# Kernel tuning notes

Hardware: AMD Instinct MI355X
Metric: run time of the kernel (lower is better)

Reference implementation:

```python
import jax, jax.numpy as jnp
import numpy as np

MIN_STD = 0.01
FOURIER_SCALE = 20.0


def _grid_sample_bilinear(h_flat, gx, gy):
    """Bilinear grid_sample with align_corners=True.
    h_flat: (N, C, H, W); gx, gy: (N, P) in [-1, 1].
    Returns (N, P, C)."""
    N, C, H, W = h_flat.shape
    x = (gx + 1.0) * 0.5 * (W - 1)
    y = (gy + 1.0) * 0.5 * (H - 1)
    x0 = jnp.clip(jnp.floor(x), 0, W - 1)
    y0 = jnp.clip(jnp.floor(y), 0, H - 1)
    x1 = jnp.clip(x0 + 1, 0, W - 1)
    y1 = jnp.clip(y0 + 1, 0, H - 1)
    wx = x - x0
    wy = y - y0
    x0i, x1i = x0.astype(jnp.int32), x1.astype(jnp.int32)
    y0i, y1i = y0.astype(jnp.int32), y1.astype(jnp.int32)
    hf = h_flat.reshape(N, C, H * W)  # flatten spatial for gather

    def gather(yi, xi):
        idx = (yi * W + xi)[:, None, :]  # (N,1,P)
        return jnp.take_along_axis(hf, idx, axis=2)  # (N,C,P)

    v00 = gather(y0i, x0i)
    v01 = gather(y0i, x1i)
    v10 = gather(y1i, x0i)
    v11 = gather(y1i, x1i)
    wx_ = wx[:, None, :]
    wy_ = wy[:, None, :]
    top = v00 * (1 - wx_) + v01 * wx_
    bot = v10 * (1 - wx_) + v11 * wx_
    out = top * (1 - wy_) + bot * wy_  # (N,C,P)
    return out.transpose(0, 2, 1)  # (N,P,C)


def setup_inputs() -> dict:
    key = jax.random.key(0)
    ks = jax.random.split(key, 9)
    B, T, C, Hg, Wg, P = 8, 16, 128, 64, 64, 2048
    h_dim, fmap = 128, 128
    in_dim = h_dim + 2 * fmap  # 384
    h_grid = jax.random.normal(ks[0], (B, T, C, Hg, Wg), dtype=jnp.float32)
    xs = jax.random.uniform(ks[1], (B, T, P, 1), dtype=jnp.float32)
    ys = jax.random.uniform(ks[2], (B, T, P, 1), dtype=jnp.float32)
    B_mat = jax.random.normal(ks[3], (2, fmap), dtype=jnp.float32) * FOURIER_SCALE
    W0 = jax.random.normal(ks[4], (in_dim, h_dim), dtype=jnp.float32) / np.sqrt(in_dim)
    b0 = jnp.zeros((h_dim,), dtype=jnp.float32)
    W1 = jax.random.normal(ks[5], (h_dim, h_dim), dtype=jnp.float32) / np.sqrt(h_dim)
    b1 = jnp.zeros((h_dim,), dtype=jnp.float32)
    W2 = jax.random.normal(ks[6], (h_dim, 2), dtype=jnp.float32) / np.sqrt(h_dim)
    b2 = jnp.zeros((2,), dtype=jnp.float32)
    return {"h_grid": h_grid, "xs": xs, "ys": ys, "B_mat": B_mat,
            "W0": W0, "b0": b0, "W1": W1, "b1": b1, "W2": W2, "b2": b2}


def reference(h_grid, xs, ys, B_mat, W0, b0, W1, b1, W2, b2):
    B, T, P, _ = xs.shape
    _, _, C, Hg, Wg = h_grid.shape
    h_flat = h_grid.reshape(B * T, C, Hg, Wg)
    coords = jnp.concatenate([xs, ys], axis=-1).reshape(B * T, P, 2)
    # map [spatial_min, spatial_max]=[0,1] to [-1,1]
    g = 2.0 * coords - 1.0
    sampled = _grid_sample_bilinear(h_flat, g[..., 0], g[..., 1])  # (BT,P,C)
    # Fourier features: [sin(2pi x B), cos(2pi x B)]
    proj = 2.0 * jnp.pi * jnp.einsum('npd,df->npf', coords, B_mat)
    spatial = jnp.concatenate([jnp.sin(proj), jnp.cos(proj)], axis=-1)  # (BT,P,256)
    x = jnp.concatenate([sampled, spatial], axis=-1)  # (BT,P,384)
    x = jax.nn.relu(x @ W0 + b0)
    x = jax.nn.relu(x @ W1 + b1)
    out = (x @ W2 + b2).reshape(B, T, P, 2)
    mu = out[..., 0:1]
    sigma = jax.nn.softplus(out[..., 1:2]) + MIN_STD
    return jnp.concatenate([mu, sigma], axis=-1)  # (B,T,P,2)
```

## Files before the change

kernel.cpp:

```cpp
#include <hip/hip_runtime.h>
#include <hip/hip_bf16.h>
#include <math.h>

typedef __attribute__((ext_vector_type(8))) short short8;
typedef __attribute__((ext_vector_type(4))) float f32x4;
typedef __attribute__((ext_vector_type(4))) unsigned short us4;

__device__ __forceinline__ float b2f(unsigned short u) {
    union { unsigned int i; float f; } v; v.i = ((unsigned int)u) << 16; return v.f;
}
__device__ __forceinline__ unsigned short f2b(float f) {
    __hip_bfloat16 h = __float2bfloat16(f);
    return *reinterpret_cast<unsigned short*>(&h);
}

__global__ __launch_bounds__(256) void transpose_h(const float* __restrict__ hg,
                                                   unsigned short* __restrict__ ht) {
    __shared__ float t[128][65];
    int bid = blockIdx.x;
    int x = bid & 7, r = bid >> 3;
    int n = x * 16 + (r & 15);
    int pb = r >> 4;
    int tid = threadIdx.x;
    const float* src = hg + (size_t)n * 128 * 4096 + pb * 64;
    int j = tid & 63, i0 = tid >> 6;
#pragma unroll
    for (int ii = 0; ii < 32; ++ii) {
        int ch = ii * 4 + i0;
        t[ch][j] = src[(size_t)ch * 4096 + j];
    }
    __syncthreads();
#pragma unroll
    for (int it = 0; it < 8; ++it) {
        int idx = tid + it * 256;
        int px = idx >> 5, cq = idx & 31;
        us4 o;
#pragma unroll
        for (int rr = 0; rr < 4; ++rr) o[rr] = f2b(t[cq * 4 + rr][px]);
        *(us4*)&ht[((size_t)n * 4096 + pb * 64 + px) * 128 + cq * 4] = o;
    }
}

__global__ void prep_weights(const float* __restrict__ W0, const float* __restrict__ W1,
                             const float* __restrict__ W2,
                             unsigned short* __restrict__ w0t, unsigned short* __restrict__ w1t,
                             unsigned short* __restrict__ w2p) {
    int i = blockIdx.x * 256 + threadIdx.x;
    const int total0 = 128 * 384, total1 = 128 * 128, total2 = 16 * 128;
    for (int idx = i; idx < total0; idx += gridDim.x * 256) {
        int j = idx / 384, k = idx - j * 384;
        w0t[idx] = f2b(W0[k * 128 + j]);
    }
    for (int idx = i; idx < total1; idx += gridDim.x * 256) {
        int j = idx >> 7, k = idx & 127;
        w1t[idx] = f2b(W1[k * 128 + j]);
    }
    for (int idx = i; idx < total2; idx += gridDim.x * 256) {
        int r = idx >> 7, k = idx & 127;
        w2p[idx] = (r < 2) ? f2b(W2[k * 2 + r]) : (unsigned short)0;
    }
}

#define W0P 784
#define HBP 272
#define MFMA_BF16 __builtin_amdgcn_mfma_f32_16x16x32_bf16

__global__ __launch_bounds__(512, 2) void fused_decoder(
    const unsigned short* __restrict__ ht,
    const float* __restrict__ xs, const float* __restrict__ ys,
    const float* __restrict__ Bm,
    const unsigned short* __restrict__ w0t, const float* __restrict__ b0,
    const unsigned short* __restrict__ w1t, const float* __restrict__ b1,
    const unsigned short* __restrict__ w2p, const float* __restrict__ b2,
    float* __restrict__ out)
{
    __shared__ char smem[128 * W0P + 8 * 16 * HBP];
    char* w0s = smem;
    int tid = threadIdx.x, lane = tid & 63, w = tid >> 6;
    int lr = lane & 15, lg = lane >> 4;
    char* hb = smem + 128 * W0P + w * 16 * HBP;

    {
        const short8* src = (const short8*)w0t;
#pragma unroll 1
        for (int it = 0; it < 12; ++it) {
            int c = tid + it * 512;
            int row = c / 48, cc = c - row * 48;
            *(short8*)(w0s + row * W0P + cc * 16) = src[c];
        }
    }
    __syncthreads();

    int bid = blockIdx.x;
    int x = bid & 7, s = bid >> 3;
    int n = x * 16 + (s >> 3);
    int pt = s & 7;
    int gp0 = n * 2048 + pt * 256 + w * 32;

    float xm[2], ym[2], wxv[2], wyv[2];
    int o00[2], o01[2], o10[2], o11[2];
#pragma unroll
    for (int m = 0; m < 2; ++m) {
        int gp = gp0 + m * 16 + lr;
        float xc = xs[gp], yc = ys[gp];
        xm[m] = xc; ym[m] = yc;
        float px = xc * 63.f, py = yc * 63.f;
        float x0f = fminf(fmaxf(floorf(px), 0.f), 63.f);
        float y0f = fminf(fmaxf(floorf(py), 0.f), 63.f);
        wxv[m] = px - x0f; wyv[m] = py - y0f;
        int xi0 = (int)x0f, yi0 = (int)y0f;
        int xi1 = min(xi0 + 1, 63), yi1 = min(yi0 + 1, 63);
        o00[m] = (yi0 * 64 + xi0) * 256;
        o01[m] = (yi0 * 64 + xi1) * 256;
        o10[m] = (yi1 * 64 + xi0) * 256;
        o11[m] = (yi1 * 64 + xi1) * 256;
    }
    const char* base = (const char*)ht + ((size_t)n << 20) + lg * 16;

    f32x4 acc[2][8];
#pragma unroll
    for (int nj = 0; nj < 8; ++nj) {
        float bv = b0[nj * 16 + lr];
        acc[0][nj] = (f32x4){bv, bv, bv, bv};
        acc[1][nj] = acc[0][nj];
    }

    short8 c00[2], c01[2], c10[2], c11[2];
#pragma unroll
    for (int m = 0; m < 2; ++m) {
        c00[m] = *(const short8*)(base + o00[m]);
        c01[m] = *(const short8*)(base + o01[m]);
        c10[m] = *(const short8*)(base + o10[m]);
        c11[m] = *(const short8*)(base + o11[m]);
    }

#pragma unroll 1
    for (int q = 0; q < 4; ++q) {
        short8 asn[2], acs[2];
        {
            int f0 = q * 32 + lg * 8;
            f32x4 B0a = *(const f32x4*)&Bm[f0];
            f32x4 B0b = *(const f32x4*)&Bm[f0 + 4];
            f32x4 B1a = *(const f32x4*)&Bm[128 + f0];
            f32x4 B1b = *(const f32x4*)&Bm[128 + f0 + 4];
#pragma unroll
            for (int m = 0; m < 2; ++m) {
                float t_[8];
#pragma unroll
                for (int j = 0; j < 4; ++j) {
                    t_[j]     = xm[m] * B0a[j] + ym[m] * B1a[j];
                    t_[4 + j] = xm[m] * B0b[j] + ym[m] * B1b[j];
                }
#pragma unroll
                for (int j = 0; j < 8; ++j) {
                    float tf = t_[j] - floorf(t_[j]);
                    float sv, cv;
                    asm("v_sin_f32 %0, %1" : "=v"(sv) : "v"(tf));
                    asm("v_cos_f32 %0, %1" : "=v"(cv) : "v"(tf));
                    asn[m][j] = (short)f2b(sv);
                    acs[m][j] = (short)f2b(cv);
                }
            }
        }
#pragma unroll
        for (int nj = 0; nj < 8; ++nj) {
            short8 bs = *(const short8*)(w0s + (nj * 16 + lr) * W0P + (4 + q) * 64 + lg * 16);
            acc[0][nj] = MFMA_BF16(asn[0], bs, acc[0][nj], 0, 0, 0);
            acc[1][nj] = MFMA_BF16(asn[1], bs, acc[1][nj], 0, 0, 0);
        }
#pragma unroll
        for (int nj = 0; nj < 8; ++nj) {
            short8 bc = *(const short8*)(w0s + (nj * 16 + lr) * W0P + (8 + q) * 64 + lg * 16);
            acc[0][nj] = MFMA_BF16(acs[0], bc, acc[0][nj], 0, 0, 0);
            acc[1][nj] = MFMA_BF16(acs[1], bc, acc[1][nj], 0, 0, 0);
        }

        short8 a[2];
#pragma unroll
        for (int m = 0; m < 2; ++m) {
            float wx = wxv[m], wy = wyv[m];
            float ivx = 1.f - wx, ivy = 1.f - wy;
#pragma unroll
            for (int j = 0; j < 8; ++j) {
                float top = b2f((unsigned short)c00[m][j]) * ivx + b2f((unsigned short)c01[m][j]) * wx;
                float bot = b2f((unsigned short)c10[m][j]) * ivx + b2f((unsigned short)c11[m][j]) * wx;
                a[m][j] = (short)f2b(top * ivy + bot * wy);
            }
        }
        if (q < 3) {
            int so = (q + 1) * 64;
#pragma unroll
            for (int m = 0; m < 2; ++m) {
                c00[m] = *(const short8*)(base + o00[m] + so);
                c01[m] = *(const short8*)(base + o01[m] + so);
                c10[m] = *(const short8*)(base + o10[m] + so);
                c11[m] = *(const short8*)(base + o11[m] + so);
            }
        }
#pragma unroll
        for (int nj = 0; nj < 8; ++nj) {
            short8 b = *(const short8*)(w0s + (nj * 16 + lr) * W0P + q * 64 + lg * 16);
            acc[0][nj] = MFMA_BF16(a[0], b, acc[0][nj], 0, 0, 0);
            acc[1][nj] = MFMA_BF16(a[1], b, acc[1][nj], 0, 0, 0);
        }
    }

    float bb2 = (lr < 2) ? b2[lr] : 0.f;
#pragma unroll
    for (int m = 0; m < 2; ++m) {
#pragma unroll
        for (int nj = 0; nj < 8; ++nj)
#pragma unroll
            for (int r = 0; r < 4; ++r) {
                int row = lg * 4 + r;
                *(unsigned short*)(hb + row * HBP + (nj * 16 + lr) * 2) =
                    f2b(fmaxf(acc[m][nj][r], 0.f));
            }
        asm volatile("s_waitcnt lgkmcnt(0)" ::: "memory");
        short8 a1[4];
#pragma unroll
        for (int ks = 0; ks < 4; ++ks)
            a1[ks] = *(const short8*)(hb + lr * HBP + ks * 64 + lg * 16);
        asm volatile("s_waitcnt lgkmcnt(0)" ::: "memory");

#pragma unroll
        for (int nj = 0; nj < 8; ++nj) {
            float bv = b1[nj * 16 + lr];
            acc[m][nj] = (f32x4){bv, bv, bv, bv};
        }
#pragma unroll
        for (int ks = 0; ks < 4; ++ks)
#pragma unroll
            for (int nj = 0; nj < 8; ++nj) {
                short8 b = *(const short8*)&w1t[(nj * 16 + lr) * 128 + ks * 32 + lg * 8];
                acc[m][nj] = MFMA_BF16(a1[ks], b, acc[m][nj], 0, 0, 0);
            }

#pragma unroll
        for (int nj = 0; nj < 8; ++nj)
#pragma unroll
            for (int r = 0; r < 4; ++r) {
                int row = lg * 4 + r;
                *(unsigned short*)(hb + row * HBP + (nj * 16 + lr) * 2) =
                    f2b(fmaxf(acc[m][nj][r], 0.f));
            }
        asm volatile("s_waitcnt lgkmcnt(0)" ::: "memory");

        f32x4 acc2 = (f32x4){bb2, bb2, bb2, bb2};
#pragma unroll
        for (int ks = 0; ks < 4; ++ks) {
            short8 a2 = *(const short8*)(hb + lr * HBP + ks * 64 + lg * 16);
            short8 bz = *(const short8*)&w2p[lr * 128 + ks * 32 + lg * 8];
            acc2 = MFMA_BF16(a2, bz, acc2, 0, 0, 0);
        }
        asm volatile("s_waitcnt lgkmcnt(0)" ::: "memory");
        if (lr < 2) {
#pragma unroll
            for (int r = 0; r < 4; ++r) {
                int gpo = gp0 + m * 16 + lg * 4 + r;
                float v = acc2[r];
                if (lr == 0) {
                    out[gpo * 2] = v;
                } else {
                    float sp = (v > 20.f) ? v : log1pf(expf(v));
                    out[gpo * 2 + 1] = sp + 0.01f;
                }
            }
        }
    }
}

extern "C" void kernel_launch(void* const* d_in, const int* in_sizes, int n_in,
                              void* d_out, int out_size, void* d_ws, size_t ws_size,
                              hipStream_t stream) {
    const float* h_grid = (const float*)d_in[0];
    const float* xs = (const float*)d_in[1];
    const float* ys = (const float*)d_in[2];
    const float* Bm = (const float*)d_in[3];
    const float* W0 = (const float*)d_in[4];
    const float* b0 = (const float*)d_in[5];
    const float* W1 = (const float*)d_in[6];
    const float* b1 = (const float*)d_in[7];
    const float* W2 = (const float*)d_in[8];
    const float* b2 = (const float*)d_in[9];
    float* out = (float*)d_out;

    unsigned short* ht  = (unsigned short*)d_ws;
    unsigned short* w0t = (unsigned short*)((char*)d_ws + 134217728ull);
    unsigned short* w1t = w0t + 128 * 384;
    unsigned short* w2p = w1t + 128 * 128;

    transpose_h<<<dim3(8192), dim3(256), 0, stream>>>(h_grid, ht);
    prep_weights<<<dim3(64), dim3(256), 0, stream>>>(W0, W1, W2, w0t, w1t, w2p);
    fused_decoder<<<dim3(1024), dim3(512), 0, stream>>>(ht, xs, ys, Bm, w0t, b0, w1t, b1, w2p, b2, out);
}
```

Baseline: 217.9 us.

## Precompute W0 projection of feature grid and split Fourier branch into separate kernel

Applies the sampled-feature block of W0 to the whole feature grid before bilinear interpolation, using the linearity of interpolation, so the decoder only interpolates projected features. The Fourier-feature part of layer 0 moves into its own kernel that writes an intermediate bf16 buffer, which the decoder adds before the ReLU. This removes the layer-0 matmul and the sin/cos work from the decoder and lowers its register and LDS use. In exchange it adds matmul work on every grid pixel and extra global-memory traffic for the intermediate buffer.

```diff
diff --git a/kernel.cpp b/kernel.cpp
--- a/kernel.cpp
+++ b/kernel.cpp
@@ -6,6 +6,8 @@
 typedef __attribute__((ext_vector_type(4))) float f32x4;
 typedef __attribute__((ext_vector_type(4))) unsigned short us4;
 
+#define MFMA_BF16 __builtin_amdgcn_mfma_f32_16x16x32_bf16
+
 __device__ __forceinline__ float b2f(unsigned short u) {
     union { unsigned int i; float f; } v; v.i = ((unsigned int)u) << 16; return v.f;
 }
@@ -14,14 +16,49 @@
     return *reinterpret_cast<unsigned short*>(&h);
 }
 
-__global__ __launch_bounds__(256) void transpose_h(const float* __restrict__ hg,
-                                                   unsigned short* __restrict__ ht) {
+__global__ void prep_weights(const float* __restrict__ W0, const float* __restrict__ W1,
+                             const float* __restrict__ W2,
+                             unsigned short* __restrict__ w0st, unsigned short* __restrict__ w0ft,
+                             unsigned short* __restrict__ w1t,  unsigned short* __restrict__ w2p) {
+    int i = blockIdx.x * 256 + threadIdx.x;
+    for (int idx = i; idx < 128 * 128; idx += gridDim.x * 256) {
+        int j = idx >> 7, k = idx & 127;
+        w0st[idx] = f2b(W0[k * 128 + j]);
+    }
+    for (int idx = i; idx < 128 * 256; idx += gridDim.x * 256) {
+        int j = idx >> 8, k = idx & 255;
+        w0ft[idx] = f2b(W0[(128 + k) * 128 + j]);
+    }
+    for (int idx = i; idx < 128 * 128; idx += gridDim.x * 256) {
+        int j = idx >> 7, k = idx & 127;
+        w1t[idx] = f2b(W1[k * 128 + j]);
+    }
+    for (int idx = i; idx < 16 * 128; idx += gridDim.x * 256) {
+        int r = idx >> 7, k = idx & 127;
+        w2p[idx] = (r < 2) ? f2b(W2[k * 2 + r]) : (unsigned short)0;
+    }
+}
+
+__global__ __launch_bounds__(256, 2) void proj_h(const float* __restrict__ hg,
+                                                 const unsigned short* __restrict__ w0st,
+                                                 unsigned short* __restrict__ P) {
     __shared__ float t[128][65];
+    __shared__ unsigned short ws[128][136];
     int bid = blockIdx.x;
     int x = bid & 7, r = bid >> 3;
     int n = x * 16 + (r & 15);
     int pb = r >> 4;
     int tid = threadIdx.x;
+
+    {
+        const short8* src = (const short8*)w0st;
+#pragma unroll
+        for (int it = 0; it < 8; ++it) {
+            int c = tid + it * 256;
+            int row = c >> 4, cc = c & 15;
+            *(short8*)&ws[row][cc * 8] = src[c];
+        }
+    }
     const float* src = hg + (size_t)n * 128 * 4096 + pb * 64;
     int j = tid & 63, i0 = tid >> 6;
 #pragma unroll
@@ -30,80 +67,164 @@
         t[ch][j] = src[(size_t)ch * 4096 + j];
     }
     __syncthreads();
+
+    int lane = tid & 63, w = tid >> 6, lr = lane & 15, lg = lane >> 4;
+    short8 afr[4];
+#pragma unroll
+    for (int ks = 0; ks < 4; ++ks) {
+        int px = w * 16 + lr;
+#pragma unroll
+        for (int jj = 0; jj < 8; ++jj)
+            afr[ks][jj] = (short)f2b(t[ks * 32 + lg * 8 + jj][px]);
+    }
+    __syncthreads();
+
+    f32x4 acc[8];
+#pragma unroll
+    for (int nj = 0; nj < 8; ++nj) acc[nj] = (f32x4){0.f, 0.f, 0.f, 0.f};
+#pragma unroll
+    for (int ks = 0; ks < 4; ++ks)
+#pragma unroll
+        for (int nj = 0; nj < 8; ++nj) {
+            short8 b = *(const short8*)&ws[nj * 16 + lr][ks * 32 + lg * 8];
+            acc[nj] = MFMA_BF16(afr[ks], b, acc[nj], 0, 0, 0);
+        }
+
+    unsigned short* tb = (unsigned short*)t;
+#pragma unroll
+    for (int nj = 0; nj < 8; ++nj)
+#pragma unroll
+        for (int r4 = 0; r4 < 4; ++r4)
+            tb[(w * 16 + lg * 4 + r4) * 136 + nj * 16 + lr] = f2b(acc[nj][r4]);
+    __syncthreads();
+    us4* dst = (us4*)(P + ((size_t)n * 4096 + pb * 64) * 128);
 #pragma unroll
     for (int it = 0; it < 8; ++it) {
         int idx = tid + it * 256;
-        int px = idx >> 5, cq = idx & 31;
-        us4 o;
-#pragma unroll
-        for (int rr = 0; rr < 4; ++rr) o[rr] = f2b(t[cq * 4 + rr][px]);
-        *(us4*)&ht[((size_t)n * 4096 + pb * 64 + px) * 128 + cq * 4] = o;
-    }
-}
-
-__global__ void prep_weights(const float* __restrict__ W0, const float* __restrict__ W1,
-                             const float* __restrict__ W2,
-                             unsigned short* __restrict__ w0t, unsigned short* __restrict__ w1t,
-                             unsigned short* __restrict__ w2p) {
-    int i = blockIdx.x * 256 + threadIdx.x;
-    const int total0 = 128 * 384, total1 = 128 * 128, total2 = 16 * 128;
-    for (int idx = i; idx < total0; idx += gridDim.x * 256) {
-        int j = idx / 384, k = idx - j * 384;
-        w0t[idx] = f2b(W0[k * 128 + j]);
-    }
-    for (int idx = i; idx < total1; idx += gridDim.x * 256) {
-        int j = idx >> 7, k = idx & 127;
-        w1t[idx] = f2b(W1[k * 128 + j]);
-    }
-    for (int idx = i; idx < total2; idx += gridDim.x * 256) {
-        int r = idx >> 7, k = idx & 127;
-        w2p[idx] = (r < 2) ? f2b(W2[k * 2 + r]) : (unsigned short)0;
-    }
-}
-
-#define W0P 784
-#define HBP 272
-#define MFMA_BF16 __builtin_amdgcn_mfma_f32_16x16x32_bf16
-
-__global__ __launch_bounds__(512, 2) void fused_decoder(
-    const unsigned short* __restrict__ ht,
+        int px = idx >> 5, c4 = idx & 31;
+        dst[px * 32 + c4] = *(us4*)&tb[px * 136 + c4 * 4];
+    }
+}
+
+__global__ __launch_bounds__(256, 3) void spatial_F(
     const float* __restrict__ xs, const float* __restrict__ ys,
-    const float* __restrict__ Bm,
-    const unsigned short* __restrict__ w0t, const float* __restrict__ b0,
+    const float* __restrict__ Bm, const unsigned short* __restrict__ w0ft,
+    const float* __restrict__ b0, unsigned short* __restrict__ F) {
+    __shared__ unsigned short hb[4][16][136];
+    int tid = threadIdx.x, lane = tid & 63, w = tid >> 6;
+    int lr = lane & 15, lg = lane >> 4;
+    int bid = blockIdx.x;
+    int x = bid & 7, s = bid >> 3;
+    int n = x * 16 + (s >> 4);
+    int gp0 = n * 2048 + (s & 15) * 128 + w * 32;
+
+    float xm[2], ym[2];
+#pragma unroll
+    for (int m = 0; m < 2; ++m) {
+        int gp = gp0 + m * 16 + lr;
+        xm[m] = xs[gp]; ym[m] = ys[gp];
+    }
+
+    f32x4 acc[2][8];
+#pragma unroll
+    for (int nj = 0; nj < 8; ++nj) {
+        float bv = b0[nj * 16 + lr];
+        acc[0][nj] = (f32x4){bv, bv, bv, bv};
+        acc[1][nj] = acc[0][nj];
+    }
+
+#pragma unroll
+    for (int ks = 0; ks < 4; ++ks) {
+        int f0 = ks * 32 + lg * 8;
+        f32x4 B0a = *(const f32x4*)&Bm[f0];
+        f32x4 B0b = *(const f32x4*)&Bm[f0 + 4];
+        f32x4 B1a = *(const f32x4*)&Bm[128 + f0];
+        f32x4 B1b = *(const f32x4*)&Bm[128 + f0 + 4];
+        short8 asn[2], acs[2];
+#pragma unroll
+        for (int m = 0; m < 2; ++m) {
+            float t_[8];
+#pragma unroll
+            for (int jj = 0; jj < 4; ++jj) {
+                t_[jj]     = xm[m] * B0a[jj] + ym[m] * B1a[jj];
+                t_[4 + jj] = xm[m] * B0b[jj] + ym[m] * B1b[jj];
+            }
+#pragma unroll
+            for (int jj = 0; jj < 8; ++jj) {
+                float tf = t_[jj] - floorf(t_[jj]);
+                float sv, cv;
+                asm("v_sin_f32 %0, %1" : "=v"(sv) : "v"(tf));
+                asm("v_cos_f32 %0, %1" : "=v"(cv) : "v"(tf));
+                asn[m][jj] = (short)f2b(sv);
+                acs[m][jj] = (short)f2b(cv);
+            }
+        }
+#pragma unroll
+        for (int nj = 0; nj < 8; ++nj) {
+            short8 bs = *(const short8*)&w0ft[(nj * 16 + lr) * 256 + ks * 32 + lg * 8];
+            acc[0][nj] = MFMA_BF16(asn[0], bs, acc[0][nj], 0, 0, 0);
+            acc[1][nj] = MFMA_BF16(asn[1], bs, acc[1][nj], 0, 0, 0);
+        }
+#pragma unroll
+        for (int nj = 0; nj < 8; ++nj) {
+            short8 bc = *(const short8*)&w0ft[(nj * 16 + lr) * 256 + (4 + ks) * 32 + lg * 8];
+            acc[0][nj] = MFMA_BF16(acs[0], bc, acc[0][nj], 0, 0, 0);
+            acc[1][nj] = MFMA_BF16(acs[1], bc, acc[1][nj], 0, 0, 0);
+        }
+    }
+
+#pragma unroll
+    for (int m = 0; m < 2; ++m) {
+#pragma unroll
+        for (int nj = 0; nj < 8; ++nj)
+#pragma unroll
+            for (int r4 = 0; r4 < 4; ++r4)
+                hb[w][lg * 4 + r4][nj * 16 + lr] = f2b(acc[m][nj][r4]);
+        asm volatile("s_waitcnt lgkmcnt(0)" ::: "memory");
+        us4* df = (us4*)(F + (size_t)(gp0 + m * 16) * 128);
+#pragma unroll
+        for (int it = 0; it < 8; ++it) {
+            int idx = lane + it * 64;
+            int px = idx >> 5, c4 = idx & 31;
+            df[px * 32 + c4] = *(us4*)&hb[w][px][c4 * 4];
+        }
+        asm volatile("s_waitcnt lgkmcnt(0)" ::: "memory");
+    }
+}
+
+__global__ __launch_bounds__(256, 3) void decoder(
+    const unsigned short* __restrict__ P, const unsigned short* __restrict__ F,
+    const float* __restrict__ xs, const float* __restrict__ ys,
     const unsigned short* __restrict__ w1t, const float* __restrict__ b1,
     const unsigned short* __restrict__ w2p, const float* __restrict__ b2,
-    float* __restrict__ out)
-{
-    __shared__ char smem[128 * W0P + 8 * 16 * HBP];
-    char* w0s = smem;
+    float* __restrict__ out) {
+    __shared__ unsigned short w1s[128][136];
+    __shared__ unsigned short hb[4][16][136];
     int tid = threadIdx.x, lane = tid & 63, w = tid >> 6;
     int lr = lane & 15, lg = lane >> 4;
-    char* hb = smem + 128 * W0P + w * 16 * HBP;
 
     {
-        const short8* src = (const short8*)w0t;
-#pragma unroll 1
-        for (int it = 0; it < 12; ++it) {
-            int c = tid + it * 512;
-            int row = c / 48, cc = c - row * 48;
-            *(short8*)(w0s + row * W0P + cc * 16) = src[c];
+        const short8* s1 = (const short8*)w1t;
+#pragma unroll
+        for (int it = 0; it < 8; ++it) {
+            int c = tid + it * 256;
+            int row = c >> 4, cc = c & 15;
+            *(short8*)&w1s[row][cc * 8] = s1[c];
         }
     }
     __syncthreads();
 
     int bid = blockIdx.x;
     int x = bid & 7, s = bid >> 3;
-    int n = x * 16 + (s >> 3);
-    int pt = s & 7;
-    int gp0 = n * 2048 + pt * 256 + w * 32;
-
-    float xm[2], ym[2], wxv[2], wyv[2];
+    int n = x * 16 + (s >> 4);
+    int gp0 = n * 2048 + (s & 15) * 128 + w * 32;
+
+    float wxv[2], wyv[2];
     int o00[2], o01[2], o10[2], o11[2];
 #pragma unroll
     for (int m = 0; m < 2; ++m) {
         int gp = gp0 + m * 16 + lr;
         float xc = xs[gp], yc = ys[gp];
-        xm[m] = xc; ym[m] = yc;
         float px = xc * 63.f, py = yc * 63.f;
         float x0f = fminf(fmaxf(floorf(px), 0.f), 63.f);
         float y0f = fminf(fmaxf(floorf(py), 0.f), 63.f);
@@ -115,95 +236,46 @@
         o10[m] = (yi1 * 64 + xi0) * 256;
         o11[m] = (yi1 * 64 + xi1) * 256;
     }
-    const char* base = (const char*)ht + ((size_t)n << 20) + lg * 16;
+    const char* base = (const char*)P + ((size_t)n << 20) + lg * 16;
+
+    short8 a1[2][4];
+#pragma unroll
+    for (int m = 0; m < 2; ++m) {
+        float wx = wxv[m], wy = wyv[m];
+        float ivx = 1.f - wx, ivy = 1.f - wy;
+        const unsigned short* fr = F + (size_t)(gp0 + m * 16 + lr) * 128 + lg * 8;
+#pragma unroll
+        for (int q = 0; q < 4; ++q) {
+            short8 c00 = *(const short8*)(base + o00[m] + q * 64);
+            short8 c01 = *(const short8*)(base + o01[m] + q * 64);
+            short8 c10 = *(const short8*)(base + o10[m] + q * 64);
+            short8 c11 = *(const short8*)(base + o11[m] + q * 64);
+            short8 f8  = *(const short8*)(fr + q * 32);
+#pragma unroll
+            for (int jj = 0; jj < 8; ++jj) {
+                float top = b2f((unsigned short)c00[jj]) * ivx + b2f((unsigned short)c01[jj]) * wx;
+                float bot = b2f((unsigned short)c10[jj]) * ivx + b2f((unsigned short)c11[jj]) * wx;
+                float v = top * ivy + bot * wy + b2f((unsigned short)f8[jj]);
+                a1[m][q][jj] = (short)f2b(fmaxf(v, 0.f));
+            }
+        }
+    }
 
     f32x4 acc[2][8];
 #pragma unroll
     for (int nj = 0; nj < 8; ++nj) {
-        float bv = b0[nj * 16 + lr];
+        float bv = b1[nj * 16 + lr];
         acc[0][nj] = (f32x4){bv, bv, bv, bv};
         acc[1][nj] = acc[0][nj];
     }
-
-    short8 c00[2], c01[2], c10[2], c11[2];
-#pragma unroll
-    for (int m = 0; m < 2; ++m) {
-        c00[m] = *(const short8*)(base + o00[m]);
-        c01[m] = *(const short8*)(base + o01[m]);
-        c10[m] = *(const short8*)(base + o10[m]);
-        c11[m] = *(const short8*)(base + o11[m]);
-    }
-
-#pragma unroll 1
-    for (int q = 0; q < 4; ++q) {
-        short8 asn[2], acs[2];
-        {
-            int f0 = q * 32 + lg * 8;
-            f32x4 B0a = *(const f32x4*)&Bm[f0];
-            f32x4 B0b = *(const f32x4*)&Bm[f0 + 4];
-            f32x4 B1a = *(const f32x4*)&Bm[128 + f0];
-            f32x4 B1b = *(const f32x4*)&Bm[128 + f0 + 4];
-#pragma unroll
-            for (int m = 0; m < 2; ++m) {
-                float t_[8];
-#pragma unroll
-                for (int j = 0; j < 4; ++j) {
-                    t_[j]     = xm[m] * B0a[j] + ym[m] * B1a[j];
-                    t_[4 + j] = xm[m] * B0b[j] + ym[m] * B1b[j];
-                }
-#pragma unroll
-                for (int j = 0; j < 8; ++j) {
-                    float tf = t_[j] - floorf(t_[j]);
-                    float sv, cv;
-                    asm("v_sin_f32 %0, %1" : "=v"(sv) : "v"(tf));
-                    asm("v_cos_f32 %0, %1" : "=v"(cv) : "v"(tf));
-                    asn[m][j] = (short)f2b(sv);
-                    acs[m][j] = (short)f2b(cv);
-                }
-            }
-        }
+#pragma unroll
+    for (int ks = 0; ks < 4; ++ks)
 #pragma unroll
         for (int nj = 0; nj < 8; ++nj) {
-            short8 bs = *(const short8*)(w0s + (nj * 16 + lr) * W0P + (4 + q) * 64 + lg * 16);
-            acc[0][nj] = MFMA_BF16(asn[0], bs, acc[0][nj], 0, 0, 0);
-            acc[1][nj] = MFMA_BF16(asn[1], bs, acc[1][nj], 0, 0, 0);
-        }
-#pragma unroll
-        for (int nj = 0; nj < 8; ++nj) {
-            short8 bc = *(const short8*)(w0s + (nj * 16 + lr) * W0P + (8 + q) * 64 + lg * 16);
-            acc[0][nj] = MFMA_BF16(acs[0], bc, acc[0][nj], 0, 0, 0);
-            acc[1][nj] = MFMA_BF16(acs[1], bc, acc[1][nj], 0, 0, 0);
-        }
-
-        short8 a[2];
-#pragma unroll
-        for (int m = 0; m < 2; ++m) {
-            float wx = wxv[m], wy = wyv[m];
-            float ivx = 1.f - wx, ivy = 1.f - wy;
-#pragma unroll
-            for (int j = 0; j < 8; ++j) {
-                float top = b2f((unsigned short)c00[m][j]) * ivx + b2f((unsigned short)c01[m][j]) * wx;
-                float bot = b2f((unsigned short)c10[m][j]) * ivx + b2f((unsigned short)c11[m][j]) * wx;
-                a[m][j] = (short)f2b(top * ivy + bot * wy);
-            }
-        }
-        if (q < 3) {
-            int so = (q + 1) * 64;
-#pragma unroll
-            for (int m = 0; m < 2; ++m) {
-                c00[m] = *(const short8*)(base + o00[m] + so);
-                c01[m] = *(const short8*)(base + o01[m] + so);
-                c10[m] = *(const short8*)(base + o10[m] + so);
-                c11[m] = *(const short8*)(base + o11[m] + so);
-            }
-        }
-#pragma unroll
-        for (int nj = 0; nj < 8; ++nj) {
-            short8 b = *(const short8*)(w0s + (nj * 16 + lr) * W0P + q * 64 + lg * 16);
-            acc[0][nj] = MFMA_BF16(a[0], b, acc[0][nj], 0, 0, 0);
-            acc[1][nj] = MFMA_BF16(a[1], b, acc[1][nj], 0, 0, 0);
-        }
-    }
+            short8 b = *(const short8*)&w1s[nj * 16 + lr][ks * 32 + lg * 8];
+            acc[0][nj] = MFMA_BF16(a1[0][ks], b, acc[0][nj], 0, 0, 0);
+            acc[1][nj] = MFMA_BF16(a1[1][ks], b, acc[1][nj], 0, 0, 0);
+        }
 
     float bb2 = (lr < 2) ? b2[lr] : 0.f;
 #pragma unroll
@@ -211,54 +283,22 @@
 #pragma unroll
         for (int nj = 0; nj < 8; ++nj)
 #pragma unroll
-            for (int r = 0; r < 4; ++r) {
-                int row = lg * 4 + r;
-                *(unsigned short*)(hb + row * HBP + (nj * 16 + lr) * 2) =
-                    f2b(fmaxf(acc[m][nj][r], 0.f));
-            }
+            for (int r4 = 0; r4 < 4; ++r4)
+                hb[w][lg * 4 + r4][nj * 16 + lr] = f2b(fmaxf(acc[m][nj][r4], 0.f));
         asm volatile("s_waitcnt lgkmcnt(0)" ::: "memory");
-        short8 a1[4];
-#pragma unroll
-        for (int ks = 0; ks < 4; ++ks)
-            a1[ks] = *(const short8*)(hb + lr * HBP + ks * 64 + lg * 16);
-        asm volatile("s_waitcnt lgkmcnt(0)" ::: "memory");
-
-#pragma unroll
-        for (int nj = 0; nj < 8; ++nj) {
-            float bv = b1[nj * 16 + lr];
-            acc[m][nj] = (f32x4){bv, bv, bv, bv};
-        }
-#pragma unroll
-        for (int ks = 0; ks < 4; ++ks)
-#pragma unroll
-            for (int nj = 0; nj < 8; ++nj) {
-                short8 b = *(const short8*)&w1t[(nj * 16 + lr) * 128 + ks * 32 + lg * 8];
-                acc[m][nj] = MFMA_BF16(a1[ks], b, acc[m][nj], 0, 0, 0);
-            }
-
-#pragma unroll
-        for (int nj = 0; nj < 8; ++nj)
-#pragma unroll
-            for (int r = 0; r < 4; ++r) {
-                int row = lg * 4 + r;
-                *(unsigned short*)(hb + row * HBP + (nj * 16 + lr) * 2) =
-                    f2b(fmaxf(acc[m][nj][r], 0.f));
-            }
-        asm volatile("s_waitcnt lgkmcnt(0)" ::: "memory");
-
         f32x4 acc2 = (f32x4){bb2, bb2, bb2, bb2};
 #pragma unroll
         for (int ks = 0; ks < 4; ++ks) {
-            short8 a2 = *(const short8*)(hb + lr * HBP + ks * 64 + lg * 16);
+            short8 a2 = *(const short8*)&hb[w][lr][ks * 32 + lg * 8];
             short8 bz = *(const short8*)&w2p[lr * 128 + ks * 32 + lg * 8];
             acc2 = MFMA_BF16(a2, bz, acc2, 0, 0, 0);
         }
         asm volatile("s_waitcnt lgkmcnt(0)" ::: "memory");
         if (lr < 2) {
 #pragma unroll
-            for (int r = 0; r < 4; ++r) {
-                int gpo = gp0 + m * 16 + lg * 4 + r;
-                float v = acc2[r];
+            for (int r4 = 0; r4 < 4; ++r4) {
+                int gpo = gp0 + m * 16 + lg * 4 + r4;
+                float v = acc2[r4];
                 if (lr == 0) {
                     out[gpo * 2] = v;
                 } else {
@@ -285,12 +325,15 @@
     const float* b2 = (const float*)d_in[9];
     float* out = (float*)d_out;
 
-    unsigned short* ht  = (unsigned short*)d_ws;
-    unsigned short* w0t = (unsigned short*)((char*)d_ws + 134217728ull);
-    unsigned short* w1t = w0t + 128 * 384;
-    unsigned short* w2p = w1t + 128 * 128;
-
-    transpose_h<<<dim3(8192), dim3(256), 0, stream>>>(h_grid, ht);
-    prep_weights<<<dim3(64), dim3(256), 0, stream>>>(W0, W1, W2, w0t, w1t, w2p);
-    fused_decoder<<<dim3(1024), dim3(512), 0, stream>>>(ht, xs, ys, Bm, w0t, b0, w1t, b1, w2p, b2, out);
-}
+    unsigned short* P    = (unsigned short*)d_ws;
+    unsigned short* F    = (unsigned short*)((char*)d_ws + 134217728ull);
+    unsigned short* w0st = (unsigned short*)((char*)d_ws + 134217728ull + 67108864ull);
+    unsigned short* w0ft = w0st + 128 * 128;
+    unsigned short* w1t  = w0ft + 128 * 256;
+    unsigned short* w2p  = w1t + 128 * 128;
+
+    prep_weights<<<dim3(64), dim3(256), 0, stream>>>(W0, W1, W2, w0st, w0ft, w1t, w2p);
+    proj_h<<<dim3(8192), dim3(256), 0, stream>>>(h_grid, w0st, P);
+    spatial_F<<<dim3(2048), dim3(256), 0, stream>>>(xs, ys, Bm, w0ft, b0, F);
+    decoder<<<dim3(2048), dim3(256), 0, stream>>>(P, F, xs, ys, w1t, b1, w2p, b2, out);
+}
```

New measurement: 300.5 us. 37.9% more time.
